# Performance work log

Measured on AMD Instinct MI355X. Metric: run time of the kernel, lower is better.

The kernel has to match this reference:

```python
import jax, jax.numpy as jnp
import numpy as np
from jax.scipy.special import logsumexp

B, S, W = 64, 128, 16
VOCAB, EMB, HID = 50000, 300, 256
CVOCAB, CEMB, CHID = 128, 50, 100
NTAGS = 50


def lstm_scan(x, Wi, Wh, b, reverse=False):
    """x: [N, T, D]. Returns (final_h [N,H], all_h [N,T,H]). Torch gate order i,f,g,o."""
    N = x.shape[0]
    H = Wh.shape[1]
    def cell(carry, xt):
        h, c = carry
        g = xt @ Wi.T + h @ Wh.T + b
        i, f, gg, o = jnp.split(g, 4, axis=-1)
        c = jax.nn.sigmoid(f) * c + jax.nn.sigmoid(i) * jnp.tanh(gg)
        h = jax.nn.sigmoid(o) * jnp.tanh(c)
        return (h, c), h
    init = (jnp.zeros((N, H), x.dtype), jnp.zeros((N, H), x.dtype))
    (hT, _), hs = jax.lax.scan(cell, init, jnp.swapaxes(x, 0, 1), reverse=reverse)
    return hT, jnp.swapaxes(hs, 0, 1)


def setup_inputs() -> dict:
    key = jax.random.key(0)
    ks = jax.random.split(key, 24)
    lengths = jnp.sort(jax.random.randint(ks[0], (B,), 1, S + 1))[::-1]
    lengths = lengths.at[0].set(S)  # pack_padded requires max length present
    valid = jnp.arange(S)[None, :] < lengths[:, None]
    sentences = jax.random.randint(ks[1], (B, S), 1, VOCAB) * valid
    tags = jax.random.randint(ks[2], (B, S), 0, NTAGS)
    words = jax.random.randint(ks[3], (B, S, W), 1, CVOCAB) * valid[:, :, None]
    def p(k, shape, scale=0.1):
        return jax.random.normal(k, shape, jnp.float32) * scale
    char_emb = p(ks[4], (CVOCAB, CEMB)).at[0].set(0.0)   # padding_idx=0
    word_emb = p(ks[5], (VOCAB, EMB)).at[0].set(0.0)     # padding_idx=0
    return dict(
        sentences=sentences.astype(jnp.int32),
        lengths=lengths.astype(jnp.int32),
        words=words.astype(jnp.int32),
        tags=tags.astype(jnp.int32),
        char_emb=char_emb,
        cWi_f=p(ks[6], (4 * CHID, CEMB)), cWh_f=p(ks[7], (4 * CHID, CHID)), cb_f=p(ks[8], (4 * CHID,)),
        cWi_b=p(ks[9], (4 * CHID, CEMB)), cWh_b=p(ks[10], (4 * CHID, CHID)), cb_b=p(ks[11], (4 * CHID,)),
        word_emb=word_emb,
        wWi_f=p(ks[12], (4 * HID, EMB + CHID)), wWh_f=p(ks[13], (4 * HID, HID)), wb_f=p(ks[14], (4 * HID,)),
        wWi_b=p(ks[15], (4 * HID, EMB + CHID)), wWh_b=p(ks[16], (4 * HID, HID)), wb_b=p(ks[17], (4 * HID,)),
        We=p(ks[18], (NTAGS, 2 * HID)), be=p(ks[19], (NTAGS,)),
        trans=jax.random.uniform(ks[20], (NTAGS, NTAGS), jnp.float32),
    )


def reference(sentences, lengths, words, tags, char_emb, cWi_f, cWh_f, cb_f,
              cWi_b, cWh_b, cb_b, word_emb, wWi_f, wWh_f, wb_f,
              wWi_b, wWh_b, wb_b, We, be, trans):
    mask = sentences != 0  # sent_pad_token = 0
    # char BiLSTM: final fwd hidden + final bwd hidden per word
    ce = char_emb[words.reshape(B * S, W)]               # [B*S, W, CEMB]
    hf, _ = lstm_scan(ce, cWi_f, cWh_f, cb_f)
    hb, _ = lstm_scan(ce, cWi_b, cWh_b, cb_b, reverse=True)
    char_enc = (hf + hb).reshape(B, S, CHID)
    x = jnp.concatenate([word_emb[sentences], char_enc], axis=-1)  # [B,S,EMB+CHID]
    # word BiLSTM with packed-sequence semantics (lengths sorted descending)
    valid = jnp.arange(S)[None, :] < lengths[:, None]
    _, h_fwd = lstm_scan(x, wWi_f, wWh_f, wb_f)
    idx = jnp.clip(lengths[:, None] - 1 - jnp.arange(S)[None, :], 0, S - 1)  # per-seq reversal
    xr = jnp.take_along_axis(x, idx[:, :, None], axis=1) * valid[:, :, None]
    _, hr = lstm_scan(xr, wWi_b, wWh_b, wb_b)
    h_bwd = jnp.take_along_axis(hr, idx[:, :, None], axis=1)
    out = jnp.concatenate([h_fwd, h_bwd], axis=-1) * valid[:, :, None]  # pad_packed zeros pads
    emit = out @ We.T + be                                # [B,S,NTAGS]
    # gold path score
    gold_emit = jnp.take_along_axis(emit, tags[:, :, None], axis=2).squeeze(-1)
    score = gold_emit.at[:, 1:].add(trans[tags[:, :-1], tags[:, 1:]])
    gold = (score * mask.astype(score.dtype)).sum(axis=1)
    # CRF forward algorithm (log partition), freezing finished sequences via mask
    def step(alpha, xs):
        e, m = xs  # e: [B,NTAGS], m: [B]
        new = logsumexp(alpha[:, :, None] + trans[None, :, :] + e[:, None, :], axis=1)
        return jnp.where(m[:, None], new, alpha), None
    alpha0 = emit[:, 0]
    alpha, _ = jax.lax.scan(step, alpha0,
                            (jnp.swapaxes(emit[:, 1:], 0, 1), mask[:, 1:].T))
    pred = logsumexp(alpha, axis=1)
    return pred - gold
```

## Files before the change

kernel.cpp:

```cpp
#include <hip/hip_runtime.h>
#include <math.h>

#define Bb 64
#define Ss 128
#define BS 8192
#define Ww 16
#define CE 50
#define CH 100
#define EMBD 300
#define HID 256
#define WG 1024
#define XD 400
#define XDP 416
#define NT 50

typedef unsigned short ushort_t;
typedef unsigned int uint_t;
using bf16x8 = __attribute__((ext_vector_type(8))) short;
using short8v = __attribute__((ext_vector_type(8))) short;
using short4v = __attribute__((ext_vector_type(4))) short;
using f32x4  = __attribute__((ext_vector_type(4))) float;
using int4v  = __attribute__((ext_vector_type(4))) int;

#define LBAR() do { asm volatile("s_waitcnt lgkmcnt(0)" ::: "memory"); __builtin_amdgcn_s_barrier(); } while(0)

__device__ __forceinline__ float sigf(float x){ return 1.0f/(1.0f+__expf(-x)); }
__device__ __forceinline__ float tanhfast(float x){
  float e = __expf(-2.0f*fabsf(x));
  float r = (1.0f-e)/(1.0f+e);
  return copysignf(r,x);
}
__device__ __forceinline__ float fsig(float x){
  float e = __builtin_amdgcn_exp2f(-1.4426950408889634f * x);
  return __builtin_amdgcn_rcpf(1.0f + e);
}
__device__ __forceinline__ float ftanh(float x){
  float e = __builtin_amdgcn_exp2f(-2.8853900817779268f * fabsf(x));
  float r = 1.0f - 2.0f*e*__builtin_amdgcn_rcpf(1.0f + e);
  return copysignf(r, x);
}
__device__ __forceinline__ ushort_t f2bf(float f){
  uint_t u = __float_as_uint(f);
  uint_t r = (u + 0x7fffu + ((u>>16)&1u)) >> 16;
  return (ushort_t)r;
}
__device__ __forceinline__ float bf2f(ushort_t u){ return __uint_as_float(((uint_t)u)<<16); }

__device__ __forceinline__ int4v sel4(int c, int4v a, int4v b){
  int4v r;
  #pragma unroll
  for (int i=0;i<4;i++) r[i] = c ? a[i] : b[i];
  return r;
}

__global__ __launch_bounds__(256) void k_cvt_whq(const float* __restrict__ whf, const float* __restrict__ whb,
                                                 signed char* __restrict__ q, float* __restrict__ dm){
  const int tid = threadIdx.x;
  const int lane = tid & 63, w = tid >> 6;
  const int gm = blockIdx.x*4 + w;
  const int dir = gm >> 10, m = gm & 1023;
  const float* src = dir ? whb : whf;
  const float* row = src + (long)((m&3)*HID + (m>>2)) * HID;
  float4 v = *(const float4*)&row[lane*4];
  float mx = fmaxf(fmaxf(fabsf(v.x), fabsf(v.y)), fmaxf(fabsf(v.z), fabsf(v.w)));
  #pragma unroll
  for (int off=32; off; off>>=1) mx = fmaxf(mx, __shfl_xor(mx, off));
  float s = (mx > 0.f) ? (127.0f / mx) : 0.f;
  int b0 = __float2int_rn(v.x*s) & 255;
  int b1 = __float2int_rn(v.y*s) & 255;
  int b2 = __float2int_rn(v.z*s) & 255;
  int b3 = __float2int_rn(v.w*s) & 255;
  uint_t pk = (uint_t)b0 | ((uint_t)b1<<8) | ((uint_t)b2<<16) | ((uint_t)b3<<24);
  *(uint_t*)&q[(long)gm*HID + lane*4] = pk;
  if (lane == 0) dm[gm] = mx * (1.0f/16129.0f);
}

__global__ __launch_bounds__(256, 2) void k_char_mfma(const int* __restrict__ words, const float* __restrict__ cemb,
    const float* __restrict__ cWiF, const float* __restrict__ cWhF, const float* __restrict__ cbF, float* __restrict__ hfo,
    const float* __restrict__ cWiB, const float* __restrict__ cWhB, const float* __restrict__ cbB, float* __restrict__ hbo)
{
  const int rev = blockIdx.y;
  const float* cWi = rev ? cWiB : cWiF;
  const float* cWh = rev ? cWhB : cWhF;
  const float* cb  = rev ? cbB  : cbF;
  float* hout = rev ? hbo : hfo;
  const int n0 = blockIdx.x * 32;
  const int tid = threadIdx.x;
  const int lane = tid & 63;
  const int w = tid >> 6;

  __shared__ ushort_t xh[32][200];
  __shared__ ushort_t wi_l[400][72];
  __shared__ float    bias_l[400];
  __shared__ int      wbuf[32][Ww];

  for (int i = tid; i < 32*Ww; i += 256)
    wbuf[i>>4][i&15] = words[(n0 + (i>>4))*Ww + (i&15)];
  for (int i = tid; i < 3200; i += 256) ((uint_t*)xh)[i] = 0u;
  for (int r = tid; r < 400; r += 256){
    int j = r >> 2, g = r & 3;
    const float* src = cWi + (g*CH + j)*CE;
    for (int k = 0; k < 72; ++k)
      wi_l[r][k] = (k < CE) ? f2bf(src[k]) : (ushort_t)0;
    bias_l[r] = cb[g*CH + j];
  }

  bf16x8 whr[7][4];
  #pragma unroll
  for (int ti=0; ti<7; ++ti){
    int tm = w + ti*4;
    #pragma unroll
    for (int kk=0; kk<4; ++kk){
      bf16x8 v;
      #pragma unroll
      for (int e=0;e<8;++e) v[e]=0;
      if (tm < 25){
        int m = tm*16 + (lane & 15);
        int j = m >> 2, g = m & 3;
        const float* src = cWh + (g*CH + j)*CH;
        int kh0 = kk*32 + ((lane>>4)<<3);
        #pragma unroll
        for (int e=0;e<8;++e){
          int kh = kh0 + e;
          if (kh < CH) v[e] = (short)f2bf(src[kh]);
        }
      }
      whr[ti][kk] = v;
    }
  }

  float cst[7][2], hreg[7][2];
  #pragma unroll
  for (int ti=0; ti<7; ++ti){ cst[ti][0]=0.f; cst[ti][1]=0.f; hreg[ti][0]=0.f; hreg[ti][1]=0.f; }

  const int ps = tid >> 3;
  const int pk = (tid & 7) * 8;
  float xv[8];

  __syncthreads();

  {
    int tt = rev ? (Ww-1) : 0;
    int wd = wbuf[ps][tt];
    const float* src = cemb + wd*CE + pk;
    #pragma unroll
    for (int e=0;e<8;++e){ int k = pk+e; xv[e] = (k < CE) ? src[e] : 0.f; }
  }

  #pragma unroll 1
  for (int t=0; t<Ww; ++t){
    __syncthreads();
    if (t){
      #pragma unroll
      for (int ti=0; ti<7; ++ti){
        int tm = w + ti*4;
        if (tm < 25){
          int j = tm*4 + (lane>>4);
          #pragma unroll
          for (int nt=0; nt<2; ++nt){
            int s = nt*16 + (lane & 15);
            xh[s][64 + j] = f2bf(hreg[ti][nt]);
          }
        }
      }
    }
    {
      bf16x8 pxv;
      #pragma unroll
      for (int e=0;e<8;++e) pxv[e] = (short)f2bf(xv[e]);
      *((bf16x8*)&xh[ps][pk]) = pxv;
    }
    if (t+1 < Ww){
      int tt2 = rev ? (Ww-2-t) : (t+1);
      int wd = wbuf[ps][tt2];
      const float* src = cemb + wd*CE + pk;
      #pragma unroll
      for (int e=0;e<8;++e){ int k = pk+e; xv[e] = (k < CE) ? src[e] : 0.f; }
    }
    __syncthreads();

    bf16x8 bf[2][6];
    #pragma unroll
    for (int nt=0; nt<2; ++nt){
      int s = nt*16 + (lane & 15);
      #pragma unroll
      for (int kk=0; kk<6; ++kk){
        int k = kk*32 + ((lane>>4)<<3);
        bf[nt][kk] = *((const bf16x8*)&xh[s][k]);
      }
    }
    #pragma unroll
    for (int ti=0; ti<7; ++ti){
      int tm = w + ti*4;
      if (tm < 25){
        int row = tm*16 + (lane & 15);
        int kb = (lane>>4)<<3;
        bf16x8 awi0 = *((const bf16x8*)&wi_l[row][kb]);
        bf16x8 awi1 = *((const bf16x8*)&wi_l[row][32+kb]);
        f32x4 bias_v = *((const f32x4*)&bias_l[tm*16 + ((lane>>4)<<2)]);
        #pragma unroll
        for (int nt=0; nt<2; ++nt){
          f32x4 acc = bias_v;
          acc = __builtin_amdgcn_mfma_f32_16x16x32_bf16(awi0, bf[nt][0], acc, 0,0,0);
          acc = __builtin_amdgcn_mfma_f32_16x16x32_bf16(awi1, bf[nt][1], acc, 0,0,0);
          #pragma unroll
          for (int kk=0; kk<4; ++kk)
            acc = __builtin_amdgcn_mfma_f32_16x16x32_bf16(whr[ti][kk], bf[nt][2+kk], acc, 0,0,0);
          float iv = sigf(acc[0]), fv = sigf(acc[1]);
          float gv = tanhfast(acc[2]), ov = sigf(acc[3]);
          float cn = fmaf(fv, cst[ti][nt], iv*gv);
          cst[ti][nt] = cn;
          hreg[ti][nt] = ov * tanhfast(cn);
        }
      }
    }
  }

  #pragma unroll
  for (int ti=0; ti<7; ++ti){
    int tm = w + ti*4;
    if (tm < 25){
      int j = tm*4 + (lane>>4);
      #pragma unroll
      for (int nt=0; nt<2; ++nt){
        int s = nt*16 + (lane & 15);
        hout[(n0 + s)*CH + j] = hreg[ti][nt];
      }
    }
  }
}

__global__ void k_build_x(const int* __restrict__ sent, const float* __restrict__ wemb,
                          const float* __restrict__ hf, const float* __restrict__ hb,
                          ushort_t* __restrict__ xbf){
  long i = (long)blockIdx.x*256 + threadIdx.x;
  if (i >= (long)BS*XDP) return;
  int n = (int)(i / XDP), e = (int)(i - (long)n*XDP);
  float v = 0.f;
  if (e < EMBD) v = wemb[(long)sent[n]*EMBD + e];
  else if (e < XD) { int jj = e-EMBD; v = hf[n*CH+jj] + hb[n*CH+jj]; }
  xbf[i] = f2bf(v);
}

__global__ void k_cvt_wi(const float* __restrict__ wiF, const float* __restrict__ wiB,
                         ushort_t* __restrict__ wiP){
  int i = blockIdx.x*256 + threadIdx.x;
  if (i >= 2*WG*XDP) return;
  int dir = i >= WG*XDP;
  int ii = dir ? i - WG*XDP : i;
  int n = ii / XDP, k = ii - n*XDP;
  const float* src = dir ? wiB : wiF;
  wiP[i] = (k < XD) ? f2bf(src[n*XD + k]) : (ushort_t)0;
}

__global__ __launch_bounds__(256) void k_gemm_mfma(const ushort_t* __restrict__ xbf, const int* __restrict__ lengths,
    const ushort_t* __restrict__ wiP, const float* __restrict__ wbF, const float* __restrict__ wbB,
    ushort_t* __restrict__ P)
{
  const int rev = blockIdx.z;
  const int b = blockIdx.x;
  const int n0 = blockIdx.y * 128;
  const float* bias = rev ? wbB : wbF;
  const int m0 = b*Ss;
  const int L = lengths[b];

  __shared__ ushort_t As[128*32];
  __shared__ ushort_t Bs[128*32];
  __shared__ float bl[128];

  const int tid = threadIdx.x;
  const int lane = tid & 63, w = tid >> 6;
  const int lo = lane & 15, hi = lane >> 4;
  const int wm0 = (w>>1)*64, wn0 = (w&1)*64;

  if (tid < 128) bl[tid] = bias[n0 + tid];

  long abase[2], bbase[2];
  #pragma unroll
  for (int u=0; u<2; ++u){
    int cid = u*256 + tid;
    int r = cid >> 2, kc = (cid & 3)*8;
    int srow;
    if (!rev) srow = m0 + r;
    else { int rr = L-1-r; srow = m0 + (rr < 0 ? 0 : rr); }
    abase[u] = (long)srow*XDP + kc;
    bbase[u] = ((long)rev*WG + n0 + r)*XDP + kc;
  }

  f32x4 acc[4][4];
  #pragma unroll
  for (int i=0;i<4;i++)
    #pragma unroll
    for (int q=0;q<4;q++){ acc[i][q][0]=0.f; acc[i][q][1]=0.f; acc[i][q][2]=0.f; acc[i][q][3]=0.f; }

  bf16x8 avn[2], bvn[2];
  #pragma unroll
  for (int u=0; u<2; ++u){
    avn[u] = *(const bf16x8*)&xbf[abase[u]];
    bvn[u] = *(const bf16x8*)&wiP[bbase[u]];
  }

  #pragma unroll 1
  for (int kt=0; kt<13; ++kt){
    bf16x8 av[2], bv[2];
    #pragma unroll
    for (int u=0; u<2; ++u){ av[u]=avn[u]; bv[u]=bvn[u]; }
    if (kt < 12){
      int k0 = (kt+1)*32;
      #pragma unroll
      for (int u=0; u<2; ++u){
        avn[u] = *(const bf16x8*)&xbf[abase[u] + k0];
        bvn[u] = *(const bf16x8*)&wiP[bbase[u] + k0];
      }
    }
    LBAR();
    #pragma unroll
    for (int u=0; u<2; ++u){
      *(bf16x8*)&As[(u*256 + tid)*8] = av[u];
      *(bf16x8*)&Bs[(u*256 + tid)*8] = bv[u];
    }
    LBAR();
    bf16x8 af[4], bfr[4];
    #pragma unroll
    for (int mt=0; mt<4; ++mt) af[mt] = *(const bf16x8*)&As[(wm0 + mt*16 + lo)*32 + hi*8];
    #pragma unroll
    for (int nt=0; nt<4; ++nt) bfr[nt] = *(const bf16x8*)&Bs[(wn0 + nt*16 + lo)*32 + hi*8];
    #pragma unroll
    for (int mt=0; mt<4; ++mt)
      #pragma unroll
      for (int nt=0; nt<4; ++nt)
        acc[mt][nt] = __builtin_amdgcn_mfma_f32_16x16x32_bf16(af[mt], bfr[nt], acc[mt][nt], 0,0,0);
  }

  LBAR();
  #pragma unroll
  for (int nt=0; nt<4; ++nt){
    int n = n0 + wn0 + nt*16 + lo;
    float bn = bl[wn0 + nt*16 + lo];
    int mp = (n & 255)*4 + (n >> 8);
    #pragma unroll
    for (int mt=0; mt<4; ++mt){
      #pragma unroll
      for (int r=0; r<4; ++r){
        int t = wm0 + mt*16 + hi*4 + r;
        long pidx = ((((long)rev*Ss + t)*16 + (b>>2))*4 + (b&3))*1024 + mp;
        P[pidx] = f2bf(acc[mt][nt][r] + bn);
      }
    }
  }
}

__global__ __launch_bounds__(512, 2) void k_word_i8(
    const signed char* __restrict__ whq, const float* __restrict__ dmg,
    const ushort_t* __restrict__ P, float* __restrict__ hfw, float* __restrict__ hrw)
{
  const int dir = blockIdx.y, sb = blockIdx.x;
  const int tid = threadIdx.x, lane = tid & 63, w = tid >> 6;
  float* hout = dir ? hrw : hfw;

  __shared__ signed char hq[2][4][320];
  if (tid < 320) ((int*)hq)[tid] = 0;

  const int hi = lane >> 4;
  const int lo = lane & 15;
  const int sq = lo & 3;
  const int g2 = lo >> 2;

  int4v wfr[8][4];
  #pragma unroll
  for (int ti=0; ti<8; ++ti){
    int mA = (w*8+ti)*16 + lo;
    #pragma unroll
    for (int kf=0; kf<4; ++kf)
      wfr[ti][kf] = *(const int4v*)&whq[(dir*1024 + mA)*HID + kf*64 + hi*16];
  }
  f32x4 dmq[2];
  #pragma unroll
  for (int u=0; u<2; ++u)
    dmq[u] = *(const f32x4*)&dmg[dir*1024 + (w*8 + g2*2+u)*16 + hi*4];

  float cst[2] = {0.f, 0.f};

  const ushort_t* Pd = P + (long)dir*8388608 + (sb*4 + sq)*1024;
  const ushort_t* gp0 = Pd + (w*8 + g2*2+0)*16 + hi*4;
  const ushort_t* gp1 = Pd + (w*8 + g2*2+1)*16 + hi*4;

  short4v gA[2], gB[2], gC[2];
  gA[0] = *(const short4v*)gp0;           gA[1] = *(const short4v*)gp1;
  gB[0] = *(const short4v*)(gp0 + 65536); gB[1] = *(const short4v*)(gp1 + 65536);

  const int j0 = (w*8 + g2*2)*4 + hi;
  const long hob = (long)(sb*4 + sq)*Ss*HID;

  int p = 0;
  __syncthreads();

  #pragma unroll 1
  for (int t=0; t<Ss; ++t){
    int t2 = (t+2 < Ss) ? (t+2) : t;
    gC[0] = *(const short4v*)(gp0 + t2*65536);
    gC[1] = *(const short4v*)(gp1 + t2*65536);

    LBAR();

    int4v bfr[4];
    #pragma unroll
    for (int kf=0; kf<4; ++kf)
      bfr[kf] = *(const int4v*)&hq[p][sq][kf*64 + hi*16];

    __builtin_amdgcn_s_setprio(1);
    int4v acc[8];
    #pragma unroll
    for (int ti=0; ti<8; ++ti){
      int4v a = {0,0,0,0};
      #pragma unroll
      for (int kf=0; kf<4; ++kf)
        a = __builtin_amdgcn_mfma_i32_16x16x64_i8(wfr[ti][kf], bfr[kf], a, 0,0,0);
      acc[ti] = a;
    }
    __builtin_amdgcn_s_setprio(0);

    #pragma unroll
    for (int u=0; u<2; ++u){
      int4v x0 = sel4(g2 & 1, acc[2+u], acc[0+u]);
      int4v x1 = sel4(g2 & 1, acc[6+u], acc[4+u]);
      int4v aS = sel4(g2 & 2, x1, x0);
      float g0v = fmaf((float)aS[0], dmq[u][0], bf2f((ushort_t)gA[u][0]));
      float g1v = fmaf((float)aS[1], dmq[u][1], bf2f((ushort_t)gA[u][1]));
      float g2v = fmaf((float)aS[2], dmq[u][2], bf2f((ushort_t)gA[u][2]));
      float g3v = fmaf((float)aS[3], dmq[u][3], bf2f((ushort_t)gA[u][3]));
      float iv = fsig(g0v), fv = fsig(g1v), gg = ftanh(g2v), ov = fsig(g3v);
      float cn = fmaf(fv, cst[u], iv*gg);
      cst[u] = cn;
      float hn = ov * ftanh(cn);
      int j = j0 + u*4;
      hout[hob + (long)t*HID + j] = hn;
      hq[1-p][sq][j] = (signed char)__float2int_rn(hn * 127.0f);
    }

    gA[0]=gB[0]; gA[1]=gB[1]; gB[0]=gC[0]; gB[1]=gC[1];
    p ^= 1;
  }
}

__global__ __launch_bounds__(128) void k_emit(const float* __restrict__ hfw, const float* __restrict__ hrw,
    const int* __restrict__ lengths, const float* __restrict__ We, const float* __restrict__ be,
    float* __restrict__ emit)
{
  __shared__ float Wl[NT*516];
  const int b = blockIdx.x, tg = blockIdx.y;
  const int tid = threadIdx.x;
  for (int i = tid; i < NT*512; i += 128)
    Wl[(i>>9)*516 + (i&511)] = We[i];
  __syncthreads();
  const int L = lengths[b];
  const int j = tid & 63;
  const int th = tid >> 6;
  float bej = (j<NT) ? be[j] : 0.f;
  for (int ttq=0; ttq<8; ttq++){
    int t = tg*16 + th*8 + ttq;
    int n = b*Ss + t;
    float acc = bej;
    if (j < NT && t < L){
      const float* hf_ = hfw + (long)n*HID;
      const float* hb_ = hrw + (long)(b*Ss + (L-1-t))*HID;
      const float* wr = Wl + j*516;
      for (int k=0;k<HID;k+=4){
        float4 hv = *(const float4*)(hf_+k);
        float4 wv = *(const float4*)(wr+k);
        acc += hv.x*wv.x + hv.y*wv.y + hv.z*wv.z + hv.w*wv.w;
      }
      for (int k=0;k<HID;k+=4){
        float4 hv = *(const float4*)(hb_+k);
        float4 wv = *(const float4*)(wr+256+k);
        acc += hv.x*wv.x + hv.y*wv.y + hv.z*wv.z + hv.w*wv.w;
      }
    }
    if (j < NT) emit[(long)n*NT + j] = acc;
  }
}

__global__ __launch_bounds__(64) void k_crf(const float* __restrict__ emit, const int* __restrict__ tags,
    const int* __restrict__ lengths, const float* __restrict__ trans, float* __restrict__ out)
{
  const int b = blockIdx.x;
  const int tid = threadIdx.x;
  __shared__ float Tl[NT*NT];
  __shared__ float A[NT];
  __shared__ float red[64];
  for (int i=tid;i<NT*NT;i+=64) Tl[i] = trans[i];
  __syncthreads();
  const int L = lengths[b];

  float gp = 0.f;
  for (int t=tid; t<L; t+=64){
    int tg = tags[b*Ss+t];
    gp += emit[(long)(b*Ss+t)*NT + tg];
    if (t>=1) gp += Tl[tags[b*Ss+t-1]*NT + tg];
  }
  red[tid] = gp; __syncthreads();
  for (int off=32; off; off>>=1){ if (tid<off) red[tid]+=red[tid+off]; __syncthreads(); }
  float gold = red[0];

  const int j = tid;
  float Ereg[NT];
  if (j < NT){
    #pragma unroll
    for (int i=0;i<NT;i++) Ereg[i] = __expf(Tl[i*NT + j]);
  }
  float a0 = (j<NT) ? emit[(long)(b*Ss)*NT + j] : -1e30f;
  float m = a0;
  #pragma unroll
  for (int off=1; off<64; off<<=1) m = fmaxf(m, __shfl_xor(m, off));
  float logZ = m;
  if (j<NT) A[j] = __expf(a0 - m);
  __syncthreads();

  for (int t=1;t<L;t++){
    float v = 0.f;
    if (j<NT){
      #pragma unroll
      for (int i=0;i<NT;i++) v = fmaf(A[i], Ereg[i], v);
      v *= __expf(emit[(long)(b*Ss+t)*NT + j]);
    }
    float mm = (j<NT) ? v : 0.f;
    #pragma unroll
    for (int off=1; off<64; off<<=1) mm = fmaxf(mm, __shfl_xor(mm, off));
    logZ += __logf(mm);
    float vn = v / mm;
    __syncthreads();
    if (j<NT) A[j] = vn;
    __syncthreads();
  }
  float s = (j<NT) ? A[j] : 0.f;
  #pragma unroll
  for (int off=1; off<64; off<<=1) s += __shfl_xor(s, off);
  float pred = logZ + __logf(s);
  if (tid==0) out[b] = pred - gold;
}

extern "C" void kernel_launch(void* const* d_in, const int* in_sizes, int n_in,
                              void* d_out, int out_size, void* d_ws, size_t ws_size,
                              hipStream_t stream){
  const int*   sentences = (const int*)d_in[0];
  const int*   lengths   = (const int*)d_in[1];
  const int*   words     = (const int*)d_in[2];
  const int*   tags      = (const int*)d_in[3];
  const float* char_emb  = (const float*)d_in[4];
  const float* cWi_f = (const float*)d_in[5];
  const float* cWh_f = (const float*)d_in[6];
  const float* cb_f  = (const float*)d_in[7];
  const float* cWi_b = (const float*)d_in[8];
  const float* cWh_b = (const float*)d_in[9];
  const float* cb_b  = (const float*)d_in[10];
  const float* word_emb = (const float*)d_in[11];
  const float* wWi_f = (const float*)d_in[12];
  const float* wWh_f = (const float*)d_in[13];
  const float* wb_f  = (const float*)d_in[14];
  const float* wWi_b = (const float*)d_in[15];
  const float* wWh_b = (const float*)d_in[16];
  const float* wb_b  = (const float*)d_in[17];
  const float* We   = (const float*)d_in[18];
  const float* be   = (const float*)d_in[19];
  const float* trans= (const float*)d_in[20];
  float* out = (float*)d_out;

  float* ws = (float*)d_ws;
  float* hf   = ws;
  float* hb   = hf  + 819200;
  float* hfw  = hb  + 819200;
  float* hrw  = hfw + 2097152;
  float* emit = hrw + 2097152;
  float* dm   = emit + 409600;
  ushort_t* xbf = (ushort_t*)(dm + 2048);
  ushort_t* wiP = xbf + 3407872;
  ushort_t* P   = wiP + 851968;
  signed char* whq = (signed char*)(P + 16777216);

  k_cvt_whq<<<dim3(512), 256, 0, stream>>>(wWh_f, wWh_b, whq, dm);
  k_cvt_wi<<<dim3(3333), 256, 0, stream>>>(wWi_f, wWi_b, wiP);
  k_char_mfma<<<dim3(256,2), 256, 0, stream>>>(words, char_emb,
      cWi_f, cWh_f, cb_f, hf,
      cWi_b, cWh_b, cb_b, hb);
  k_build_x<<<dim3(13312), 256, 0, stream>>>(sentences, word_emb, hf, hb, xbf);
  k_gemm_mfma<<<dim3(64,8,2), 256, 0, stream>>>(xbf, lengths, wiP, wb_f, wb_b, P);
  k_word_i8<<<dim3(16,2), 512, 0, stream>>>(whq, dm, P, hfw, hrw);
  k_emit<<<dim3(64,8), 128, 0, stream>>>(hfw, hrw, lengths, We, be, emit);
  k_crf<<<dim3(64), 64, 0, stream>>>(emit, tags, lengths, trans, out);
}
```

Measured before the change: 465.2 us.

## Restructure char LSTM kernel: 512 threads, fused Wh|Wi K dimension, register-resident weights

The character BiLSTM kernel moves from 256 to 512 threads per block, and the input and recurrent weights are concatenated into one 150-wide K dimension (padded to 160). Each wave keeps three 16-row tiles of that combined weight in registers, and the 25th tile is served from LDS by the last wave. This cuts the MFMA count per tile from six to five and removes the per-step LDS reads of Wi. Activations switch to exp2/rcp intrinsics, and barriers become LBAR. The risk is load imbalance on wave 7, which does extra work each step, plus higher register pressure under launch_bounds(512,4).

New measurement: 471.0 us. About the same (+1.2%).

```diff
diff --git a/kernel.cpp b/kernel.cpp
--- a/kernel.cpp
+++ b/kernel.cpp
@@ -13,6 +13,7 @@
 #define XD 400
 #define XDP 416
 #define NT 50
+#define KS 168
 
 typedef unsigned short ushort_t;
 typedef unsigned int uint_t;
@@ -24,12 +25,6 @@
 
 #define LBAR() do { asm volatile("s_waitcnt lgkmcnt(0)" ::: "memory"); __builtin_amdgcn_s_barrier(); } while(0)
 
-__device__ __forceinline__ float sigf(float x){ return 1.0f/(1.0f+__expf(-x)); }
-__device__ __forceinline__ float tanhfast(float x){
-  float e = __expf(-2.0f*fabsf(x));
-  float r = (1.0f-e)/(1.0f+e);
-  return copysignf(r,x);
-}
 __device__ __forceinline__ float fsig(float x){
   float e = __builtin_amdgcn_exp2f(-1.4426950408889634f * x);
   return __builtin_amdgcn_rcpf(1.0f + e);
@@ -75,7 +70,7 @@
   if (lane == 0) dm[gm] = mx * (1.0f/16129.0f);
 }
 
-__global__ __launch_bounds__(256, 2) void k_char_mfma(const int* __restrict__ words, const float* __restrict__ cemb,
+__global__ __launch_bounds__(512, 4) void k_char_mfma(const int* __restrict__ words, const float* __restrict__ cemb,
     const float* __restrict__ cWiF, const float* __restrict__ cWhF, const float* __restrict__ cbF, float* __restrict__ hfo,
     const float* __restrict__ cWiB, const float* __restrict__ cWhB, const float* __restrict__ cbB, float* __restrict__ hbo)
 {
@@ -88,145 +83,146 @@
   const int tid = threadIdx.x;
   const int lane = tid & 63;
   const int w = tid >> 6;
-
-  __shared__ ushort_t xh[32][200];
-  __shared__ ushort_t wi_l[400][72];
-  __shared__ float    bias_l[400];
-  __shared__ int      wbuf[32][Ww];
-
-  for (int i = tid; i < 32*Ww; i += 256)
+  const int lo = lane & 15, hi = lane >> 4;
+
+  __shared__ ushort_t xh[32][KS];
+  __shared__ ushort_t wt24[16][KS];
+  __shared__ float bias_l[400];
+  __shared__ int wbuf[32][Ww];
+
+  for (int i = tid; i < 32*Ww; i += 512)
     wbuf[i>>4][i&15] = words[(n0 + (i>>4))*Ww + (i&15)];
-  for (int i = tid; i < 3200; i += 256) ((uint_t*)xh)[i] = 0u;
-  for (int r = tid; r < 400; r += 256){
-    int j = r >> 2, g = r & 3;
-    const float* src = cWi + (g*CH + j)*CE;
-    for (int k = 0; k < 72; ++k)
-      wi_l[r][k] = (k < CE) ? f2bf(src[k]) : (ushort_t)0;
-    bias_l[r] = cb[g*CH + j];
-  }
-
-  bf16x8 whr[7][4];
-  #pragma unroll
-  for (int ti=0; ti<7; ++ti){
-    int tm = w + ti*4;
-    #pragma unroll
-    for (int kk=0; kk<4; ++kk){
+  for (int i = tid; i < 32*KS/2; i += 512) ((uint_t*)xh)[i] = 0u;
+  for (int i = tid; i < 400; i += 512) bias_l[i] = cb[(i&3)*CH + (i>>2)];
+  for (int i = tid; i < 16*KS; i += 512){
+    int rr = i / KS, k = i - rr*KS;
+    int m = 384 + rr, j = m>>2, g = m&3;
+    float v = 0.f;
+    if (k < CH) v = cWh[(g*CH+j)*CH + k];
+    else if (k < CH+CE) v = cWi[(g*CH+j)*CE + (k-CH)];
+    wt24[rr][k] = f2bf(v);
+  }
+
+  bf16x8 wc[3][5];
+  #pragma unroll
+  for (int ti=0; ti<3; ++ti){
+    int m = (w*3+ti)*16 + lo;
+    int j = m>>2, g = m&3;
+    const float* whrow = cWh + (g*CH+j)*CH;
+    const float* wirow = cWi + (g*CH+j)*CE;
+    #pragma unroll
+    for (int kk=0; kk<5; ++kk){
       bf16x8 v;
       #pragma unroll
-      for (int e=0;e<8;++e) v[e]=0;
-      if (tm < 25){
-        int m = tm*16 + (lane & 15);
-        int j = m >> 2, g = m & 3;
-        const float* src = cWh + (g*CH + j)*CH;
-        int kh0 = kk*32 + ((lane>>4)<<3);
-        #pragma unroll
-        for (int e=0;e<8;++e){
-          int kh = kh0 + e;
-          if (kh < CH) v[e] = (short)f2bf(src[kh]);
-        }
-      }
-      whr[ti][kk] = v;
-    }
-  }
-
-  float cst[7][2], hreg[7][2];
-  #pragma unroll
-  for (int ti=0; ti<7; ++ti){ cst[ti][0]=0.f; cst[ti][1]=0.f; hreg[ti][0]=0.f; hreg[ti][1]=0.f; }
-
-  const int ps = tid >> 3;
-  const int pk = (tid & 7) * 8;
-  float xv[8];
+      for (int e=0;e<8;++e){
+        int k = kk*32 + hi*8 + e;
+        float f = 0.f;
+        if (k < CH) f = whrow[k];
+        else if (k < CH+CE) f = wirow[k-CH];
+        v[e] = (short)f2bf(f);
+      }
+      wc[ti][kk] = v;
+    }
+  }
+
+  float cst[3][2], hreg[3][2], cst4[2], hreg4[2];
+  #pragma unroll
+  for (int ti=0; ti<3; ++ti){ cst[ti][0]=0.f; cst[ti][1]=0.f; hreg[ti][0]=0.f; hreg[ti][1]=0.f; }
+  cst4[0]=0.f; cst4[1]=0.f; hreg4[0]=0.f; hreg4[1]=0.f;
+
+  const int ps = tid >> 4;
+  const int e0 = (tid & 15) * 4;
+  float xp[4];
 
   __syncthreads();
 
   {
     int tt = rev ? (Ww-1) : 0;
     int wd = wbuf[ps][tt];
-    const float* src = cemb + wd*CE + pk;
-    #pragma unroll
-    for (int e=0;e<8;++e){ int k = pk+e; xv[e] = (k < CE) ? src[e] : 0.f; }
+    #pragma unroll
+    for (int q=0;q<4;++q){ int e = e0+q; xp[q] = (e < CE) ? cemb[wd*CE + e] : 0.f; }
   }
 
   #pragma unroll 1
   for (int t=0; t<Ww; ++t){
-    __syncthreads();
+    LBAR();
     if (t){
       #pragma unroll
-      for (int ti=0; ti<7; ++ti){
-        int tm = w + ti*4;
-        if (tm < 25){
-          int j = tm*4 + (lane>>4);
-          #pragma unroll
-          for (int nt=0; nt<2; ++nt){
-            int s = nt*16 + (lane & 15);
-            xh[s][64 + j] = f2bf(hreg[ti][nt]);
-          }
-        }
-      }
-    }
-    {
-      bf16x8 pxv;
-      #pragma unroll
-      for (int e=0;e<8;++e) pxv[e] = (short)f2bf(xv[e]);
-      *((bf16x8*)&xh[ps][pk]) = pxv;
+      for (int ti=0; ti<3; ++ti){
+        int j = (w*3+ti)*4 + hi;
+        #pragma unroll
+        for (int nt=0; nt<2; ++nt)
+          xh[nt*16+lo][j] = f2bf(hreg[ti][nt]);
+      }
+      if (w == 7){
+        #pragma unroll
+        for (int nt=0; nt<2; ++nt)
+          xh[nt*16+lo][96+hi] = f2bf(hreg4[nt]);
+      }
+    }
+    if (e0 < 48){
+      short4v pv;
+      #pragma unroll
+      for (int q=0;q<4;++q) pv[q] = (short)f2bf(xp[q]);
+      *(short4v*)&xh[ps][CH + e0] = pv;
+    } else if (e0 == 48){
+      xh[ps][CH+48] = f2bf(xp[0]);
+      xh[ps][CH+49] = f2bf(xp[1]);
     }
     if (t+1 < Ww){
       int tt2 = rev ? (Ww-2-t) : (t+1);
       int wd = wbuf[ps][tt2];
-      const float* src = cemb + wd*CE + pk;
-      #pragma unroll
-      for (int e=0;e<8;++e){ int k = pk+e; xv[e] = (k < CE) ? src[e] : 0.f; }
-    }
-    __syncthreads();
-
-    bf16x8 bf[2][6];
+      #pragma unroll
+      for (int q=0;q<4;++q){ int e = e0+q; xp[q] = (e < CE) ? cemb[wd*CE + e] : 0.f; }
+    }
+    LBAR();
+
     #pragma unroll
     for (int nt=0; nt<2; ++nt){
-      int s = nt*16 + (lane & 15);
-      #pragma unroll
-      for (int kk=0; kk<6; ++kk){
-        int k = kk*32 + ((lane>>4)<<3);
-        bf[nt][kk] = *((const bf16x8*)&xh[s][k]);
-      }
-    }
-    #pragma unroll
-    for (int ti=0; ti<7; ++ti){
-      int tm = w + ti*4;
-      if (tm < 25){
-        int row = tm*16 + (lane & 15);
-        int kb = (lane>>4)<<3;
-        bf16x8 awi0 = *((const bf16x8*)&wi_l[row][kb]);
-        bf16x8 awi1 = *((const bf16x8*)&wi_l[row][32+kb]);
-        f32x4 bias_v = *((const f32x4*)&bias_l[tm*16 + ((lane>>4)<<2)]);
+      int s = nt*16 + lo;
+      bf16x8 bfr[5];
+      #pragma unroll
+      for (int kk=0; kk<5; ++kk)
+        bfr[kk] = *((const bf16x8*)&xh[s][kk*32 + hi*8]);
+      #pragma unroll
+      for (int ti=0; ti<3; ++ti){
+        f32x4 acc = *((const f32x4*)&bias_l[(w*3+ti)*16 + hi*4]);
         #pragma unroll
-        for (int nt=0; nt<2; ++nt){
-          f32x4 acc = bias_v;
-          acc = __builtin_amdgcn_mfma_f32_16x16x32_bf16(awi0, bf[nt][0], acc, 0,0,0);
-          acc = __builtin_amdgcn_mfma_f32_16x16x32_bf16(awi1, bf[nt][1], acc, 0,0,0);
-          #pragma unroll
-          for (int kk=0; kk<4; ++kk)
-            acc = __builtin_amdgcn_mfma_f32_16x16x32_bf16(whr[ti][kk], bf[nt][2+kk], acc, 0,0,0);
-          float iv = sigf(acc[0]), fv = sigf(acc[1]);
-          float gv = tanhfast(acc[2]), ov = sigf(acc[3]);
-          float cn = fmaf(fv, cst[ti][nt], iv*gv);
-          cst[ti][nt] = cn;
-          hreg[ti][nt] = ov * tanhfast(cn);
+        for (int kk=0; kk<5; ++kk)
+          acc = __builtin_amdgcn_mfma_f32_16x16x32_bf16(wc[ti][kk], bfr[kk], acc, 0,0,0);
+        float iv = fsig(acc[0]), fv = fsig(acc[1]);
+        float gv = ftanh(acc[2]), ov = fsig(acc[3]);
+        float cn = fmaf(fv, cst[ti][nt], iv*gv);
+        cst[ti][nt] = cn;
+        hreg[ti][nt] = ov * ftanh(cn);
+      }
+      if (w == 7){
+        f32x4 acc = *((const f32x4*)&bias_l[384 + hi*4]);
+        #pragma unroll
+        for (int kk=0; kk<5; ++kk){
+          bf16x8 at = *((const bf16x8*)&wt24[lo][kk*32 + hi*8]);
+          acc = __builtin_amdgcn_mfma_f32_16x16x32_bf16(at, bfr[kk], acc, 0,0,0);
         }
-      }
-    }
-  }
-
-  #pragma unroll
-  for (int ti=0; ti<7; ++ti){
-    int tm = w + ti*4;
-    if (tm < 25){
-      int j = tm*4 + (lane>>4);
-      #pragma unroll
-      for (int nt=0; nt<2; ++nt){
-        int s = nt*16 + (lane & 15);
-        hout[(n0 + s)*CH + j] = hreg[ti][nt];
-      }
-    }
+        float iv = fsig(acc[0]), fv = fsig(acc[1]);
+        float gv = ftanh(acc[2]), ov = fsig(acc[3]);
+        float cn = fmaf(fv, cst4[nt], iv*gv);
+        cst4[nt] = cn;
+        hreg4[nt] = ov * ftanh(cn);
+      }
+    }
+  }
+
+  #pragma unroll
+  for (int ti=0; ti<3; ++ti){
+    int j = (w*3+ti)*4 + hi;
+    #pragma unroll
+    for (int nt=0; nt<2; ++nt)
+      hout[(n0 + nt*16 + lo)*CH + j] = hreg[ti][nt];
+  }
+  if (w == 7){
+    #pragma unroll
+    for (int nt=0; nt<2; ++nt)
+      hout[(n0 + nt*16 + lo)*CH + 96 + hi] = hreg4[nt];
   }
 }
 
@@ -579,7 +575,7 @@
 
   k_cvt_whq<<<dim3(512), 256, 0, stream>>>(wWh_f, wWh_b, whq, dm);
   k_cvt_wi<<<dim3(3333), 256, 0, stream>>>(wWi_f, wWi_b, wiP);
-  k_char_mfma<<<dim3(256,2), 256, 0, stream>>>(words, char_emb,
+  k_char_mfma<<<dim3(256,2), 512, 0, stream>>>(words, char_emb,
       cWi_f, cWh_f, cb_f, hf,
       cWi_b, cWh_b, cb_b, hb);
   k_build_x<<<dim3(13312), 256, 0, stream>>>(sentences, word_emb, hf, hb, xbf);
```
